# Kernel tuning notes

Hardware: AMD Instinct MI355X
Metric: run time of the kernel (lower is better)

Reference implementation:

```python
import jax, jax.numpy as jnp
import numpy as np

N = 50000          # nodes
E = 800000         # edges (avg degree 16)
IN, H, OUT = 128, 256, 128
K = 100            # low-rank attention rank (hard-coded self.k = 100)
BN_EPS = 1e-5


def _lin(key, din, dout):
    return jax.random.normal(key, (din, dout), jnp.float32) / np.sqrt(din)


def setup_inputs() -> dict:
    key = jax.random.key(0)
    ks = jax.random.split(key, 16)
    inp = {
        "x": jax.random.normal(ks[0], (N, IN), jnp.float32),
        "edge_index": jax.random.randint(ks[1], (2, E), 0, N, jnp.int32),
    }
    dins = [IN, H, H]
    douts = [H, H, OUT]
    j = 2
    for i, (di, do) in enumerate(zip(dins, douts)):
        inp[f"cw{i}"] = _lin(ks[j], di, H); j += 1          # GCNConv weight
        inp[f"cb{i}"] = jnp.zeros((H,), jnp.float32)          # GCNConv bias
        inp[f"aw{i}"] = _lin(ks[j], di, 4 * K); j += 1        # attention U|V|Z|T projection
        inp[f"ab{i}"] = jnp.zeros((4 * K,), jnp.float32)
        inp[f"rw{i}"] = _lin(ks[j], 2 * K + H, do); j += 1    # dimension_reduce linear
        inp[f"rb{i}"] = jnp.zeros((do,), jnp.float32)
    for i in range(2):                                        # BN for first num_layers-1 blocks
        inp[f"g{i}"] = jnp.ones((H,), jnp.float32)
        inp[f"bt{i}"] = jnp.zeros((H,), jnp.float32)
    return inp


def _gcn(x, W, b, src, dst):
    n = x.shape[0]
    loops = jnp.arange(n, dtype=src.dtype)
    s = jnp.concatenate([src, loops])
    d = jnp.concatenate([dst, loops])
    deg = jax.ops.segment_sum(jnp.ones(d.shape, x.dtype), d, num_segments=n)
    dis = jax.lax.rsqrt(jnp.maximum(deg, 1.0))  # deg >= 1 due to self loops
    h = x @ W                                    # [N, H]
    msg = h[s] * (dis[s] * dis[d])[:, None]      # [E+N, H]
    return jax.ops.segment_sum(msg, d, num_segments=n) + b


def _lowrank(x, Aw, Ab):
    # LowRankAttention: tmp = relu(x W); split into U,V,Z,T of width K each.
    t = jax.nn.relu(x @ Aw + Ab)                 # [N, 4K]
    U, V, Z, T = t[:, :K], t[:, K:2 * K], t[:, 2 * K:3 * K], t[:, 3 * K:]
    n = x.shape[0]
    # joint_normalize2: scalar norm factor
    nf = jnp.sum(U @ (V.T @ jnp.ones((n, 1), x.dtype))) / n + 1e-6
    res = U @ (V.T @ Z)                          # low-rank global attention [N, K]
    return jnp.concatenate([res / nf, T], axis=1)  # [N, 2K]


def _bn(x, g, b):
    m = jnp.mean(x, axis=0)
    v = jnp.var(x, axis=0)
    return (x - m) * jax.lax.rsqrt(v + BN_EPS) * g + b


def reference(x, edge_index, cw0, cb0, aw0, ab0, rw0, rb0, g0, bt0,
              cw1, cb1, aw1, ab1, rw1, rb1, g1, bt1,
              cw2, cb2, aw2, ab2, rw2, rb2):
    src, dst = edge_index[0], edge_index[1]
    layers = [(cw0, cb0, aw0, ab0, rw0, rb0, g0, bt0),
              (cw1, cb1, aw1, ab1, rw1, rb1, g1, bt1)]
    for cw, cb, aw, ab, rw, rb, g, bt in layers:
        x_local = jax.nn.relu(_gcn(x, cw, cb, src, dst))  # dropout p=0 (eval)
        x_global = _lowrank(x, aw, ab)
        x = jax.nn.relu(jnp.concatenate([x_global, x_local], axis=1) @ rw + rb)
        x = _bn(x, g, bt)
    x_local = jax.nn.relu(_gcn(x, cw2, cb2, src, dst))
    x_global = _lowrank(x, aw2, ab2)
    return jnp.concatenate([x_global, x_local], axis=1) @ rw2 + rb2
```

## Files before the change

### kernel.cpp

```cpp
#include <hip/hip_runtime.h>

typedef _Float16 f16;
typedef __attribute__((ext_vector_type(8))) _Float16 f16x8;
typedef __attribute__((ext_vector_type(4))) _Float16 f16x4;
typedef __attribute__((ext_vector_type(2))) _Float16 f16x2;
typedef __attribute__((ext_vector_type(4))) float f32x4;

#define LDA2 72

__global__ __launch_bounds__(256, 2) void gemm2(
    const f16* __restrict__ A, int lda,
    const f16* __restrict__ Bt, int Kd,
    const float* __restrict__ bias,
    f16* __restrict__ Cb, float* __restrict__ Cf, int ldc,
    int R, int ncols, int relu,
    float* __restrict__ csbuf,
    float* __restrict__ bnsum_ptr,
    f16* __restrict__ hbD, f16* __restrict__ tbufD, f16* __restrict__ xcatD,
    int mode)
{
    __shared__ f16 As[256 * LDA2];
    __shared__ f16 Bs[128 * LDA2];
    const int tid  = threadIdx.x;
    const int wid  = tid >> 6;
    const int lane = tid & 63;
    const int m    = lane & 15;
    const int quad = lane >> 4;

    const long rowblk = (long)blockIdx.x * 256;
    const long row0   = rowblk + wid * 64;
    const int  colbase = blockIdx.y * 128;

    f32x4 acc[4][8];
#pragma unroll
    for (int rt = 0; rt < 4; ++rt)
#pragma unroll
        for (int ct = 0; ct < 8; ++ct)
            acc[rt][ct] = f32x4{0.f, 0.f, 0.f, 0.f};

    for (int k0 = 0; k0 < Kd; k0 += 64) {
        const int BK = (Kd - k0 >= 64) ? 64 : (Kd - k0);
        const int sb = (BK == 64) ? 3 : 2;
        const int smask = (1 << sb) - 1;
        if (k0) __syncthreads();
        const int itA = BK >> 3;
        for (int i = 0; i < itA; ++i) {
            int u = i * 256 + tid;
            int r = u >> sb, s = u & smask;
            long rr = rowblk + r; if (rr > (long)R - 1) rr = (long)R - 1;
            *(f16x8*)&As[r * LDA2 + s * 8] = *(const f16x8*)(A + rr * (long)lda + k0 + s * 8);
        }
        const int itB = BK >> 4;
        for (int i = 0; i < itB; ++i) {
            int u = i * 256 + tid;
            int c = u >> sb, s = u & smask;
            *(f16x8*)&Bs[c * LDA2 + s * 8] =
                *(const f16x8*)(Bt + (long)(colbase + c) * Kd + k0 + s * 8);
        }
        __syncthreads();
#pragma unroll 2
        for (int kk = 0; kk < BK; kk += 32) {
            f16x8 a[4], b[8];
#pragma unroll
            for (int rt = 0; rt < 4; ++rt)
                a[rt] = *(const f16x8*)&As[(wid * 64 + rt * 16 + m) * LDA2 + kk + quad * 8];
#pragma unroll
            for (int ct = 0; ct < 8; ++ct)
                b[ct] = *(const f16x8*)&Bs[(ct * 16 + m) * LDA2 + kk + quad * 8];
#pragma unroll
            for (int ct = 0; ct < 8; ++ct)
#pragma unroll
                for (int rt = 0; rt < 4; ++rt)
                    acc[rt][ct] = __builtin_amdgcn_mfma_f32_16x16x32_f16(a[rt], b[ct], acc[rt][ct], 0, 0, 0);
        }
    }

    float rsum[8], rsq[8];
#pragma unroll
    for (int ct = 0; ct < 8; ++ct) { rsum[ct] = 0.f; rsq[ct] = 0.f; }

    if (mode == 1) {
#pragma unroll
        for (int ct = 0; ct < 8; ++ct) {
            int col = colbase + ct * 16 + m;
            if (col >= 656) continue;
            float bv = bias[col];
            bool isrelu = col >= 256;
            f16* dst; int ldc2, c2;
            if (col < 256)      { dst = hbD;   ldc2 = 256; c2 = col; }
            else if (col < 556) { dst = tbufD; ldc2 = 300; c2 = col - 256; }
            else                { dst = xcatD; ldc2 = 456; c2 = col - 556; }
#pragma unroll
            for (int rt = 0; rt < 4; ++rt) {
#pragma unroll
                for (int r = 0; r < 4; ++r) {
                    long row = row0 + rt * 16 + quad * 4 + r;
                    if (row < R) {
                        float v = acc[rt][ct][r] + bv;
                        if (isrelu && v < 0.f) v = 0.f;
                        dst[row * (long)ldc2 + c2] = (f16)v;
                        rsum[ct] += v;
                    }
                }
            }
        }
        if (colbase == 256 || colbase == 384) {
            __syncthreads();
            float* scr = (float*)Bs;
#pragma unroll
            for (int ct = 0; ct < 8; ++ct) {
                float s = rsum[ct];
                s += __shfl_xor(s, 16);
                s += __shfl_xor(s, 32);
                if (quad == 0) scr[wid * 128 + ct * 16 + m] = s;
            }
            __syncthreads();
            if (tid < 128) {
                int gcol = colbase + tid;
                if (gcol < 456) {
                    float s = scr[tid] + scr[128 + tid] + scr[256 + tid] + scr[384 + tid];
                    atomicAdd(&csbuf[gcol - 256], s);
                }
            }
        }
    } else {
#pragma unroll
        for (int ct = 0; ct < 8; ++ct) {
            int col = colbase + ct * 16 + m;
            if (col >= ncols) continue;
            float bv = bias ? bias[col] : 0.f;
#pragma unroll
            for (int rt = 0; rt < 4; ++rt) {
#pragma unroll
                for (int r = 0; r < 4; ++r) {
                    long row = row0 + rt * 16 + quad * 4 + r;
                    if (row < R) {
                        float v = acc[rt][ct][r] + bv;
                        if (relu && v < 0.f) v = 0.f;
                        if (Cf) Cf[row * (long)ldc + col] = v;
                        else    Cb[row * (long)ldc + col] = (f16)v;
                        rsum[ct] += v;
                        rsq[ct]  += v * v;
                    }
                }
            }
        }
        if (bnsum_ptr) {
            __syncthreads();
            float* scr = (float*)Bs;
#pragma unroll
            for (int ct = 0; ct < 8; ++ct) {
                float s = rsum[ct];
                s += __shfl_xor(s, 16);
                s += __shfl_xor(s, 32);
                float q = rsq[ct];
                q += __shfl_xor(q, 16);
                q += __shfl_xor(q, 32);
                if (quad == 0) {
                    scr[wid * 128 + ct * 16 + m]       = s;
                    scr[512 + wid * 128 + ct * 16 + m] = q;
                }
            }
            __syncthreads();
            if (tid < 128) {
                int col = colbase + tid;
                if (col < ncols) {
                    float s = scr[tid] + scr[128 + tid] + scr[256 + tid] + scr[384 + tid];
                    float q = scr[512 + tid] + scr[640 + tid] + scr[768 + tid] + scr[896 + tid];
                    atomicAdd(&bnsum_ptr[col], s);
                    atomicAdd(&bnsum_ptr[256 + col], q);
                }
            }
        }
    }
}

struct PrepJobs {
    const float* src[13];
    void*        dst[13];
    int   K[13], ncols[13], Kd[13], type[13];
    long  start[13], elems[13];
    int   njobs;
};

__global__ __launch_bounds__(256) void prep_all(PrepJobs J)
{
    long b = blockIdx.x;
    int j = 0;
    for (int i = 1; i < J.njobs; ++i)
        if (b >= J.start[i]) j = i;
    long idx = (b - J.start[j]) * 256 + threadIdx.x;
    if (idx >= J.elems[j]) return;
    int ty = J.type[j];
    if (ty == 0) {
        int Kd = J.Kd[j];
        int k = (int)(idx % Kd);
        long n = idx / Kd;
        float v = (k < J.K[j] && n < J.ncols[j]) ? J.src[j][(long)k * J.ncols[j] + n] : 0.f;
        ((f16*)J.dst[j])[idx] = (f16)v;
    } else if (ty == 1) {
        ((f16*)J.dst[j])[idx] = (f16)J.src[j][idx];
    } else if (ty == 2) {
        ((float*)J.dst[j])[idx] = 0.f;
    } else {
        float v = (idx >= 256 && idx < 656) ? J.src[j][idx - 256] : 0.f;
        ((float*)J.dst[j])[idx] = v;
    }
}

__global__ void hist_kernel(const int* __restrict__ dst, int E, int* __restrict__ cnt)
{
    int e = blockIdx.x * 256 + threadIdx.x;
    if (e < E) atomicAdd(&cnt[dst[e]], 1);
}

__global__ __launch_bounds__(1024) void scanA_kernel(const int* __restrict__ cnt, int n,
                                                     int* __restrict__ csum)
{
    __shared__ int sdata[1024];
    int t = threadIdx.x;
    int i = blockIdx.x * 1024 + t;
    sdata[t] = (i < n) ? cnt[i] : 0;
    __syncthreads();
    for (int d = 512; d > 0; d >>= 1) {
        if (t < d) sdata[t] += sdata[t + d];
        __syncthreads();
    }
    if (t == 0) csum[blockIdx.x] = sdata[0];
}

__global__ void scanB_kernel(int* __restrict__ csum, int nchunks, int n, int* __restrict__ rowptr)
{
    if (threadIdx.x == 0) {
        int run = 0;
        for (int b = 0; b < nchunks; ++b) {
            int v = csum[b];
            csum[b] = run;
            run += v;
        }
        rowptr[n] = run;
    }
}

__global__ __launch_bounds__(1024) void scanC_kernel(const int* __restrict__ cnt, int n,
                                                     const int* __restrict__ csum,
                                                     int* __restrict__ rowptr,
                                                     int* __restrict__ cursor,
                                                     float* __restrict__ dis)
{
    __shared__ int sdata[1024];
    int t = threadIdx.x;
    int i = blockIdx.x * 1024 + t;
    int v = (i < n) ? cnt[i] : 0;
    sdata[t] = v;
    __syncthreads();
    for (int d = 1; d < 1024; d <<= 1) {
        int x = (t >= d) ? sdata[t - d] : 0;
        __syncthreads();
        sdata[t] += x;
        __syncthreads();
    }
    if (i < n) {
        int excl = csum[blockIdx.x] + sdata[t] - v;
        rowptr[i] = excl;
        cursor[i] = excl;
        dis[i] = rsqrtf((float)(v + 1));
    }
}

__global__ void scatter_kernel(const int* __restrict__ src, const int* __restrict__ dst,
                               int E, int* __restrict__ cursor, int* __restrict__ colidx)
{
    int e = blockIdx.x * 256 + threadIdx.x;
    if (e < E) {
        int d = dst[e];
        int pos = atomicAdd(&cursor[d], 1);
        colidx[pos] = src[e];
    }
}

__global__ __launch_bounds__(256) void agg_kernel(
    const f16* __restrict__ h, const int* __restrict__ rowptr,
    const int* __restrict__ colidx, const float* __restrict__ dis,
    const float* __restrict__ cb, f16* __restrict__ out, int ldc, int R)
{
    int wid = threadIdx.x >> 6, lane = threadIdx.x & 63;
    int i = blockIdx.x * 4 + wid;
    if (i >= R) return;
    float disi = dis[i];
    f16x4 hv = *(const f16x4*)(h + (long)i * 256 + lane * 4);
    float acc[4];
#pragma unroll
    for (int j = 0; j < 4; ++j) acc[j] = (float)hv[j] * disi;
    int e0 = rowptr[i], e1 = rowptr[i + 1];
    int e = e0;
    for (; e + 3 < e1; e += 4) {
        int s0 = colidx[e], s1 = colidx[e + 1], s2 = colidx[e + 2], s3 = colidx[e + 3];
        float w0 = dis[s0], w1 = dis[s1], w2 = dis[s2], w3 = dis[s3];
        f16x4 h0 = *(const f16x4*)(h + (long)s0 * 256 + lane * 4);
        f16x4 h1 = *(const f16x4*)(h + (long)s1 * 256 + lane * 4);
        f16x4 h2 = *(const f16x4*)(h + (long)s2 * 256 + lane * 4);
        f16x4 h3 = *(const f16x4*)(h + (long)s3 * 256 + lane * 4);
#pragma unroll
        for (int j = 0; j < 4; ++j)
            acc[j] += (float)h0[j] * w0 + (float)h1[j] * w1
                    + (float)h2[j] * w2 + (float)h3[j] * w3;
    }
    for (; e < e1; ++e) {
        int s = colidx[e];
        float w = dis[s];
        f16x4 hs = *(const f16x4*)(h + (long)s * 256 + lane * 4);
#pragma unroll
        for (int j = 0; j < 4; ++j) acc[j] += (float)hs[j] * w;
    }
    f16x4 o;
#pragma unroll
    for (int j = 0; j < 4; ++j) {
        float v = acc[j] * disi + cb[lane * 4 + j];
        if (v < 0.f) v = 0.f;
        o[j] = (f16)v;
    }
    *(f16x4*)(out + (long)i * ldc + lane * 4) = o;
}

#define VTZ_BLOCKS 192
__global__ __launch_bounds__(256) void vtz_mfma(const f16* __restrict__ t, int ld, int R,
                                                float* __restrict__ Mpart)
{
    __shared__ f16 Vt[112 * 72];
    __shared__ f16 Zt[112 * 72];
    const int tid  = threadIdx.x;
    const int wid  = tid >> 6;
    const int lane = tid & 63;
    const int m    = lane & 15;
    const int quad = lane >> 4;

    for (int idx = tid; idx < 12 * 64; idx += 256) {
        int c = 100 + (idx >> 6), r = idx & 63;
        Vt[c * 72 + r] = (f16)0.f;
        Zt[c * 72 + r] = (f16)0.f;
    }

    f32x4 acc[2][7];
#pragma unroll
    for (int rt = 0; rt < 2; ++rt)
#pragma unroll
        for (int ct = 0; ct < 7; ++ct)
            acc[rt][ct] = f32x4{0.f, 0.f, 0.f, 0.f};

    for (long base = (long)blockIdx.x * 64; base < R; base += (long)gridDim.x * 64) {
        __syncthreads();
        for (int idx = tid; idx < 50 * 64; idx += 256) {
            int r = idx / 50, c2 = (idx - r * 50) * 2;
            f16x2 v2 = f16x2{(f16)0.f, (f16)0.f};
            f16x2 z2 = f16x2{(f16)0.f, (f16)0.f};
            if (base + r < R) {
                v2 = *(const f16x2*)(t + (base + r) * ld + 100 + c2);
                z2 = *(const f16x2*)(t + (base + r) * ld + 200 + c2);
            }
            Vt[c2 * 72 + r] = v2[0]; Vt[(c2 + 1) * 72 + r] = v2[1];
            Zt[c2 * 72 + r] = z2[0]; Zt[(c2 + 1) * 72 + r] = z2[1];
        }
        __syncthreads();
#pragma unroll
        for (int ks = 0; ks < 2; ++ks) {
            int k0 = ks * 32 + quad * 8;
            f16x8 b[7];
#pragma unroll
            for (int ct = 0; ct < 7; ++ct)
                b[ct] = *(const f16x8*)&Zt[(ct * 16 + m) * 72 + k0];
#pragma unroll
            for (int rt = 0; rt < 2; ++rt) {
                int tr = wid + rt * 4;
                if (tr >= 7) continue;
                f16x8 a = *(const f16x8*)&Vt[(tr * 16 + m) * 72 + k0];
#pragma unroll
                for (int ct = 0; ct < 7; ++ct)
                    acc[rt][ct] = __builtin_amdgcn_mfma_f32_16x16x32_f16(a, b[ct], acc[rt][ct], 0, 0, 0);
            }
        }
    }

    float* out = Mpart + (long)blockIdx.x * 10000;
#pragma unroll
    for (int rt = 0; rt < 2; ++rt) {
        int tr = wid + rt * 4;
        if (tr >= 7) continue;
#pragma unroll
        for (int ct = 0; ct < 7; ++ct) {
            int b = ct * 16 + m;
            if (b >= 100) continue;
#pragma unroll
            for (int r = 0; r < 4; ++r) {
                int a = tr * 16 + quad * 4 + r;
                if (a < 100) out[a * 100 + b] = acc[rt][ct][r];
            }
        }
    }
}

__global__ __launch_bounds__(256) void vtz_reduce2(const float* __restrict__ Mpart,
                                                   f16* __restrict__ MT,
                                                   const float* __restrict__ cs, int R)
{
    __shared__ float s2[256];
    int t = threadIdx.x;
    float v = (t < 100) ? cs[t] * cs[100 + t] : 0.f;
    s2[t] = v;
    __syncthreads();
    for (int d = 128; d > 0; d >>= 1) {
        if (t < d) s2[t] += s2[t + d];
        __syncthreads();
    }
    float scale = 1.0f / (s2[0] / (float)R + 1e-6f);

    int idx = blockIdx.x * 256 + t;
    if (idx >= 10000) return;
    float s = 0.f;
    for (int b = 0; b < VTZ_BLOCKS; ++b) s += Mpart[(long)b * 10000 + idx];
    s *= scale;
    int a = idx / 100, c = idx - a * 100;
    MT[c * 128 + a] = (f16)s;
}

__global__ __launch_bounds__(256) void bn_fold2(
    f16* __restrict__ bigBT,
    const float* __restrict__ cwf, const float* __restrict__ awf,
    const float* __restrict__ bnsum, const float* __restrict__ g,
    const float* __restrict__ bt, int R,
    const float* __restrict__ ab0, float* __restrict__ biascat)
{
    __shared__ float a_s[256], b_s[256];
    const int t = threadIdx.x;
    {
        float s0 = bnsum[t];
        float s1 = bnsum[256 + t];
        float mean = s0 / (float)R;
        float var  = s1 / (float)R - mean * mean;
        if (var < 0.f) var = 0.f;
        float a = g[t] * rsqrtf(var + 1e-5f);
        a_s[t] = a;
        b_s[t] = bt[t] - mean * a;
    }
    __syncthreads();
    const int bid = blockIdx.x;
    if (bid < 768) {
        long idx = (long)bid * 256 + t;
        bigBT[idx] = (f16)((float)bigBT[idx] * a_s[t]);
    } else if (bid == 768) {
        float s = 0.f;
        for (int k = 0; k < 256; ++k) s += b_s[k] * cwf[(long)k * 256 + t];
        biascat[t] = s;
    } else {
        int n = (bid - 769) * 256 + t;
        if (n < 400) {
            float s = ab0[n];
            for (int k = 0; k < 256; ++k) s += b_s[k] * awf[(long)k * 400 + n];
            biascat[256 + n] = s;
        }
    }
}

extern "C" void kernel_launch(void* const* d_in, const int* in_sizes, int n_in,
                              void* d_out, int out_size, void* d_ws, size_t ws_size,
                              hipStream_t stream)
{
    (void)n_in; (void)out_size; (void)ws_size;
    const int N = in_sizes[0] / 128;
    const int E = in_sizes[1] / 2;

    const float* x0 = (const float*)d_in[0];
    const int*  ei   = (const int*)d_in[1];
    const int*  esrc = ei;
    const int*  edst = ei + E;
    const float *cw[3], *cbv[3], *aw[3], *abv[3], *rw[3], *rbv[3];
    for (int l = 0; l < 3; ++l) {
        cw[l]  = (const float*)d_in[2 + 6 * l];
        cbv[l] = (const float*)d_in[3 + 6 * l];
        aw[l]  = (const float*)d_in[4 + 6 * l];
        abv[l] = (const float*)d_in[5 + 6 * l];
        rw[l]  = (const float*)d_in[6 + 6 * l];
        rbv[l] = (const float*)d_in[7 + 6 * l];
    }
    const float* g[2]   = {(const float*)d_in[20], (const float*)d_in[22]};
    const float* btb[2] = {(const float*)d_in[21], (const float*)d_in[23]};

    char* p = (char*)d_ws;
    auto carve = [&](size_t bytes) -> char* {
        char* r = p; p += (bytes + 255) & ~(size_t)255; return r;
    };
    int*   cnt    = (int*)carve((size_t)N * 4);
    int*   rowptr = (int*)carve((size_t)(N + 1) * 4);
    int*   cursor = (int*)carve((size_t)N * 4);
    int*   colidx = (int*)carve((size_t)E * 4);
    float* dis    = (float*)carve((size_t)N * 4);
    int*   csum   = (int*)carve(256 * 4);
    float* Mpart  = (float*)carve((size_t)VTZ_BLOCKS * 10000 * 4);
    float* zr     = (float*)carve(9984 * 4);
    float* csbufL[3] = {zr, zr + 256, zr + 512};
    float* bnsumA = zr + 768;
    float* bnsumB = zr + 1280;
    f16*   MT     = (f16*)(zr + 1792);
    float* biascat = (float*)carve(768 * 4);
    f16*   bigBT[3], *rwT[3];
    int din[3] = {128, 256, 256};
    int dou[3] = {256, 256, 128};
    for (int l = 0; l < 3; ++l) {
        bigBT[l] = (f16*)carve((size_t)768 * din[l] * 2);
        rwT[l]   = (f16*)carve((size_t)dou[l] * 480 * 2);
    }
    f16*   xbf  = (f16*)carve((size_t)N * 256 * 2);
    float* hbuf = (float*)carve((size_t)N * 256 * 4);
    f16*   hb   = (f16*)hbuf;
    f16*   tbuf = (f16*)carve((size_t)N * 300 * 2);
    f16*   xcat = (f16*)carve(((size_t)N * 456 + 32) * 2);

    PrepJobs J{};
    int nj = 0; long blk = 0;
    auto addJob = [&](const float* s, void* d, int K, int nc, int Kd, int ty, long elems) {
        J.src[nj] = s; J.dst[nj] = d; J.K[nj] = K; J.ncols[nj] = nc; J.Kd[nj] = Kd;
        J.type[nj] = ty; J.start[nj] = blk; J.elems[nj] = elems;
        blk += (elems + 255) / 256; ++nj;
    };
    for (int l = 0; l < 3; ++l)
        addJob(cw[l], bigBT[l], din[l], 256, din[l], 0, (long)256 * din[l]);
    for (int l = 0; l < 3; ++l)
        addJob(aw[l], bigBT[l] + (long)256 * din[l], din[l], 400, din[l], 0, (long)512 * din[l]);
    for (int l = 0; l < 3; ++l)
        addJob(rw[l], rwT[l], 456, dou[l], 480, 0, (long)dou[l] * 480);
    addJob(x0, xbf, 0, 0, 0, 1, (long)N * 128);
    addJob(nullptr, zr, 0, 0, 0, 2, 9984);
    addJob(nullptr, cnt, 0, 0, 0, 2, N);
    addJob(abv[0], biascat, 0, 0, 0, 3, 768);
    J.njobs = nj;

    prep_all<<<(unsigned)blk, 256, 0, stream>>>(J);

    const int nchunks = (N + 1023) / 1024;
    hist_kernel<<<(E + 255) / 256, 256, 0, stream>>>(edst, E, cnt);
    scanA_kernel<<<nchunks, 1024, 0, stream>>>(cnt, N, csum);
    scanB_kernel<<<1, 64, 0, stream>>>(csum, nchunks, N, rowptr);
    scanC_kernel<<<nchunks, 1024, 0, stream>>>(cnt, N, csum, rowptr, cursor, dis);
    scatter_kernel<<<(E + 255) / 256, 256, 0, stream>>>(esrc, edst, E, cursor, colidx);

    int lda = 128;
    const unsigned gx2 = (unsigned)((N + 255) / 256);

    for (int l = 0; l < 3; ++l) {
        float* bnsumX = (l == 0) ? bnsumA : bnsumB;

        gemm2<<<dim3(gx2, 6), 256, 0, stream>>>(xbf, lda, bigBT[l], din[l], biascat,
                                                nullptr, nullptr, 0, N, 656, 0,
                                                csbufL[l], nullptr,
                                                hb, tbuf, xcat + 100, 1);
        vtz_mfma<<<VTZ_BLOCKS, 256, 0, stream>>>(tbuf, 300, N, Mpart);
        vtz_reduce2<<<40, 256, 0, stream>>>(Mpart, MT, csbufL[l], N);
        gemm2<<<dim3(gx2, 1), 256, 0, stream>>>(tbuf, 300, MT, 128, nullptr,
                                                xcat, nullptr, 456, N, 100, 0,
                                                nullptr, nullptr,
                                                nullptr, nullptr, nullptr, 0);
        agg_kernel<<<(N + 3) / 4, 256, 0, stream>>>(hb, rowptr, colidx, dis, cbv[l],
                                                    xcat + 200, 456, N);
        if (l < 2) {
            gemm2<<<dim3(gx2, 2), 256, 0, stream>>>(xcat, 456, rwT[l], 480, rbv[l],
                                                    xbf, nullptr, 256, N, 256, 1,
                                                    nullptr, bnsumX,
                                                    nullptr, nullptr, nullptr, 0);
            bn_fold2<<<771, 256, 0, stream>>>(bigBT[l + 1], cw[l + 1], aw[l + 1],
                                              bnsumX, g[l], btb[l], N,
                                              abv[l + 1], biascat);
            lda = 256;
        } else {
            gemm2<<<dim3(gx2, 1), 256, 0, stream>>>(xcat, 456, rwT[l], 480, rbv[l],
                                                    nullptr, (float*)d_out, 128, N, 128, 0,
                                                    nullptr, nullptr,
                                                    nullptr, nullptr, nullptr, 0);
        }
    }
}
```

Before: 980.2 us.

## Register-prefetch GEMM K-tiles and stage epilogue through LDS for vector stores

The GEMM kernel now works on 32-wide K tiles. While the current tile's MFMAs run, the next tile's global loads are already in flight in registers, a register-level software pipeline. The f16 output epilogue first writes results to a per-wave LDS tile, then issues coalesced 4-wide vector stores instead of scattered scalar 2-byte stores. Shared memory is reorganised into one 70KB buffer and the min-blocks launch bound is dropped, which may lower occupancy and add register pressure.

```diff
diff --git a/kernel.cpp b/kernel.cpp
--- a/kernel.cpp
+++ b/kernel.cpp
@@ -6,9 +6,7 @@
 typedef __attribute__((ext_vector_type(2))) _Float16 f16x2;
 typedef __attribute__((ext_vector_type(4))) float f32x4;
 
-#define LDA2 72
-
-__global__ __launch_bounds__(256, 2) void gemm2(
+__global__ __launch_bounds__(256) void gemm3(
     const f16* __restrict__ A, int lda,
     const f16* __restrict__ Bt, int Kd,
     const float* __restrict__ bias,
@@ -19,8 +17,11 @@
     f16* __restrict__ hbD, f16* __restrict__ tbufD, f16* __restrict__ xcatD,
     int mode)
 {
-    __shared__ f16 As[256 * LDA2];
-    __shared__ f16 Bs[128 * LDA2];
+    __shared__ char smem[71680];
+    f16* As = (f16*)smem;
+    f16* Bs = (f16*)(smem + 20480);
+    float* scr = (float*)(smem + 67584);
+
     const int tid  = threadIdx.x;
     const int wid  = tid >> 6;
     const int lane = tid & 63;
@@ -38,58 +39,69 @@
         for (int ct = 0; ct < 8; ++ct)
             acc[rt][ct] = f32x4{0.f, 0.f, 0.f, 0.f};
 
-    for (int k0 = 0; k0 < Kd; k0 += 64) {
-        const int BK = (Kd - k0 >= 64) ? 64 : (Kd - k0);
-        const int sb = (BK == 64) ? 3 : 2;
-        const int smask = (1 << sb) - 1;
+    const f16* pA[4]; f16* wA[4];
+    const f16* pB[2]; f16* wB[2];
+#pragma unroll
+    for (int i = 0; i < 4; ++i) {
+        int u = i * 256 + tid;
+        int r = u >> 2, s = u & 3;
+        long rr = rowblk + r; if (rr > (long)R - 1) rr = (long)R - 1;
+        pA[i] = A + rr * (long)lda + s * 8;
+        wA[i] = &As[r * 40 + s * 8];
+    }
+#pragma unroll
+    for (int i = 0; i < 2; ++i) {
+        int u = i * 256 + tid;
+        int c = u >> 2, s = u & 3;
+        pB[i] = Bt + (long)(colbase + c) * Kd + s * 8;
+        wB[i] = &Bs[c * 40 + s * 8];
+    }
+
+    f16x8 ra[4], rb[2];
+#pragma unroll
+    for (int i = 0; i < 4; ++i) ra[i] = *(const f16x8*)(pA[i]);
+#pragma unroll
+    for (int i = 0; i < 2; ++i) rb[i] = *(const f16x8*)(pB[i]);
+
+    for (int k0 = 0; k0 < Kd; k0 += 32) {
         if (k0) __syncthreads();
-        const int itA = BK >> 3;
-        for (int i = 0; i < itA; ++i) {
-            int u = i * 256 + tid;
-            int r = u >> sb, s = u & smask;
-            long rr = rowblk + r; if (rr > (long)R - 1) rr = (long)R - 1;
-            *(f16x8*)&As[r * LDA2 + s * 8] = *(const f16x8*)(A + rr * (long)lda + k0 + s * 8);
-        }
-        const int itB = BK >> 4;
-        for (int i = 0; i < itB; ++i) {
-            int u = i * 256 + tid;
-            int c = u >> sb, s = u & smask;
-            *(f16x8*)&Bs[c * LDA2 + s * 8] =
-                *(const f16x8*)(Bt + (long)(colbase + c) * Kd + k0 + s * 8);
-        }
+#pragma unroll
+        for (int i = 0; i < 4; ++i) *(f16x8*)wA[i] = ra[i];
+#pragma unroll
+        for (int i = 0; i < 2; ++i) *(f16x8*)wB[i] = rb[i];
         __syncthreads();
-#pragma unroll 2
-        for (int kk = 0; kk < BK; kk += 32) {
-            f16x8 a[4], b[8];
+        if (k0 + 32 < Kd) {
+#pragma unroll
+            for (int i = 0; i < 4; ++i) ra[i] = *(const f16x8*)(pA[i] + k0 + 32);
+#pragma unroll
+            for (int i = 0; i < 2; ++i) rb[i] = *(const f16x8*)(pB[i] + k0 + 32);
+        }
+        f16x8 a[4], b[8];
+#pragma unroll
+        for (int rt = 0; rt < 4; ++rt)
+            a[rt] = *(const f16x8*)&As[(wid * 64 + rt * 16 + m) * 40 + quad * 8];
+#pragma unroll
+        for (int ct = 0; ct < 8; ++ct)
+            b[ct] = *(const f16x8*)&Bs[(ct * 16 + m) * 40 + quad * 8];
+#pragma unroll
+        for (int ct = 0; ct < 8; ++ct)
 #pragma unroll
             for (int rt = 0; rt < 4; ++rt)
-                a[rt] = *(const f16x8*)&As[(wid * 64 + rt * 16 + m) * LDA2 + kk + quad * 8];
-#pragma unroll
-            for (int ct = 0; ct < 8; ++ct)
-                b[ct] = *(const f16x8*)&Bs[(ct * 16 + m) * LDA2 + kk + quad * 8];
-#pragma unroll
-            for (int ct = 0; ct < 8; ++ct)
-#pragma unroll
-                for (int rt = 0; rt < 4; ++rt)
-                    acc[rt][ct] = __builtin_amdgcn_mfma_f32_16x16x32_f16(a[rt], b[ct], acc[rt][ct], 0, 0, 0);
-        }
-    }
+                acc[rt][ct] = __builtin_amdgcn_mfma_f32_16x16x32_f16(a[rt], b[ct], acc[rt][ct], 0, 0, 0);
+    }
+
+    __syncthreads();
 
     float rsum[8], rsq[8];
 #pragma unroll
     for (int ct = 0; ct < 8; ++ct) { rsum[ct] = 0.f; rsq[ct] = 0.f; }
 
-    if (mode == 1) {
+    if (mode == 0 && Cf) {
 #pragma unroll
         for (int ct = 0; ct < 8; ++ct) {
             int col = colbase + ct * 16 + m;
-            if (col >= 656) continue;
-            float bv = bias[col];
-            bool isrelu = col >= 256;
-            f16* dst; int ldc2, c2;
-            if (col < 256)      { dst = hbD;   ldc2 = 256; c2 = col; }
-            else if (col < 556) { dst = tbufD; ldc2 = 300; c2 = col - 256; }
-            else                { dst = xcatD; ldc2 = 456; c2 = col - 556; }
+            if (col >= ncols) continue;
+            float bv = bias ? bias[col] : 0.f;
 #pragma unroll
             for (int rt = 0; rt < 4; ++rt) {
 #pragma unroll
@@ -97,16 +109,58 @@
                     long row = row0 + rt * 16 + quad * 4 + r;
                     if (row < R) {
                         float v = acc[rt][ct][r] + bv;
-                        if (isrelu && v < 0.f) v = 0.f;
-                        dst[row * (long)ldc2 + c2] = (f16)v;
-                        rsum[ct] += v;
+                        if (relu && v < 0.f) v = 0.f;
+                        Cf[row * (long)ldc + col] = v;
                     }
                 }
             }
         }
+        return;
+    }
+
+    f16* epw = (f16*)smem + wid * (64 * 132);
+
+    if (mode == 1) {
+#pragma unroll
+        for (int ct = 0; ct < 8; ++ct) {
+            int col = colbase + ct * 16 + m;
+            float bv = bias[col];
+            bool isrelu = col >= 256;
+#pragma unroll
+            for (int rt = 0; rt < 4; ++rt) {
+#pragma unroll
+                for (int r = 0; r < 4; ++r) {
+                    long row = row0 + rt * 16 + quad * 4 + r;
+                    float v = acc[rt][ct][r] + bv;
+                    if (isrelu && v < 0.f) v = 0.f;
+                    if (row < R) rsum[ct] += v;
+                    epw[(rt * 16 + quad * 4 + r) * 132 + ct * 16 + m] = (f16)v;
+                }
+            }
+        }
+#pragma unroll
+        for (int it = 0; it < 16; ++it) {
+            int rl = it * 4 + (lane >> 4);
+            int ch = lane & 15;
+            long grow = rowblk + wid * 64 + rl;
+            if (grow >= R) continue;
+            f16x4 v0 = *(const f16x4*)&epw[rl * 132 + ch * 8];
+            f16x4 v1 = *(const f16x4*)&epw[rl * 132 + ch * 8 + 4];
+            int cg = colbase + ch * 8;
+#pragma unroll
+            for (int h = 0; h < 2; ++h) {
+                int c4 = cg + h * 4;
+                f16x4 vv = h ? v1 : v0;
+                f16* dst; int ld2, c2;
+                if (c4 < 256)      { dst = hbD;   ld2 = 256; c2 = c4; }
+                else if (c4 < 556) { dst = tbufD; ld2 = 300; c2 = c4 - 256; }
+                else if (c4 < 656) { dst = xcatD; ld2 = 456; c2 = c4 - 556; }
+                else continue;
+                *(f16x4*)&dst[grow * (long)ld2 + c2] = vv;
+            }
+        }
         if (colbase == 256 || colbase == 384) {
             __syncthreads();
-            float* scr = (float*)Bs;
 #pragma unroll
             for (int ct = 0; ct < 8; ++ct) {
                 float s = rsum[ct];
@@ -127,27 +181,40 @@
 #pragma unroll
         for (int ct = 0; ct < 8; ++ct) {
             int col = colbase + ct * 16 + m;
-            if (col >= ncols) continue;
-            float bv = bias ? bias[col] : 0.f;
+            float bv = (bias && col < ncols) ? bias[col] : 0.f;
 #pragma unroll
             for (int rt = 0; rt < 4; ++rt) {
 #pragma unroll
                 for (int r = 0; r < 4; ++r) {
                     long row = row0 + rt * 16 + quad * 4 + r;
-                    if (row < R) {
-                        float v = acc[rt][ct][r] + bv;
-                        if (relu && v < 0.f) v = 0.f;
-                        if (Cf) Cf[row * (long)ldc + col] = v;
-                        else    Cb[row * (long)ldc + col] = (f16)v;
+                    float v = acc[rt][ct][r] + bv;
+                    if (relu && v < 0.f) v = 0.f;
+                    if (col < ncols && row < R) {
                         rsum[ct] += v;
                         rsq[ct]  += v * v;
                     }
+                    epw[(rt * 16 + quad * 4 + r) * 132 + ct * 16 + m] = (f16)v;
                 }
+            }
+        }
+#pragma unroll
+        for (int it = 0; it < 16; ++it) {
+            int rl = it * 4 + (lane >> 4);
+            int ch = lane & 15;
+            long grow = rowblk + wid * 64 + rl;
+            if (grow >= R) continue;
+            f16x4 v0 = *(const f16x4*)&epw[rl * 132 + ch * 8];
+            f16x4 v1 = *(const f16x4*)&epw[rl * 132 + ch * 8 + 4];
+            int cg = colbase + ch * 8;
+#pragma unroll
+            for (int h = 0; h < 2; ++h) {
+                int c4 = cg + h * 4;
+                if (c4 < ncols)
+                    *(f16x4*)&Cb[grow * (long)ldc + c4] = h ? v1 : v0;
             }
         }
         if (bnsum_ptr) {
             __syncthreads();
-            float* scr = (float*)Bs;
 #pragma unroll
             for (int ct = 0; ct < 8; ++ct) {
                 float s = rsum[ct];
@@ -549,20 +616,20 @@
     for (int l = 0; l < 3; ++l) {
         float* bnsumX = (l == 0) ? bnsumA : bnsumB;
 
-        gemm2<<<dim3(gx2, 6), 256, 0, stream>>>(xbf, lda, bigBT[l], din[l], biascat,
+        gemm3<<<dim3(gx2, 6), 256, 0, stream>>>(xbf, lda, bigBT[l], din[l], biascat,
                                                 nullptr, nullptr, 0, N, 656, 0,
                                                 csbufL[l], nullptr,
                                                 hb, tbuf, xcat + 100, 1);
         vtz_mfma<<<VTZ_BLOCKS, 256, 0, stream>>>(tbuf, 300, N, Mpart);
         vtz_reduce2<<<40, 256, 0, stream>>>(Mpart, MT, csbufL[l], N);
-        gemm2<<<dim3(gx2, 1), 256, 0, stream>>>(tbuf, 300, MT, 128, nullptr,
+        gemm3<<<dim3(gx2, 1), 256, 0, stream>>>(tbuf, 300, MT, 128, nullptr,
                                                 xcat, nullptr, 456, N, 100, 0,
                                                 nullptr, nullptr,
                                                 nullptr, nullptr, nullptr, 0);
         agg_kernel<<<(N + 3) / 4, 256, 0, stream>>>(hb, rowptr, colidx, dis, cbv[l],
                                                     xcat + 200, 456, N);
         if (l < 2) {
-            gemm2<<<dim3(gx2, 2), 256, 0, stream>>>(xcat, 456, rwT[l], 480, rbv[l],
+            gemm3<<<dim3(gx2, 2), 256, 0, stream>>>(xcat, 456, rwT[l], 480, rbv[l],
                                                     xbf, nullptr, 256, N, 256, 1,
                                                     nullptr, bnsumX,
                                                     nullptr, nullptr, nullptr, 0);
@@ -571,7 +638,7 @@
                                               abv[l + 1], biascat);
             lda = 256;
         } else {
-            gemm2<<<dim3(gx2, 1), 256, 0, stream>>>(xcat, 456, rwT[l], 480, rbv[l],
+            gemm3<<<dim3(gx2, 1), 256, 0, stream>>>(xcat, 456, rwT[l], 480, rbv[l],
                                                     nullptr, (float*)d_out, 128, N, 128, 0,
                                                     nullptr, nullptr,
                                                     nullptr, nullptr, nullptr, 0);
```

Result: no change. 962.3 us (-1.8%).

## Shrink GEMM tile to 128x128 with 2x2 warp grid and LDS-staged vector stores

Applied to the files above, without the earlier changes.

Replaces the 256x128 GEMM tile with a 128x128 tile split across a 2x2 arrangement of waves, halving accumulator registers and LDS so launch bounds can allow four blocks per CU, with twice as many blocks in the grid. The f16 epilogue now stages results through shared memory and writes 4-wide vector stores instead of scattered scalar stores. The column-sum and BN-statistic reductions are adapted to the new layout. The cost is lower data reuse per block, more redundant B-tile loads, and an extra LDS round trip in the epilogue.

```diff
diff --git a/kernel.cpp b/kernel.cpp
--- a/kernel.cpp
+++ b/kernel.cpp
@@ -6,9 +6,7 @@
 typedef __attribute__((ext_vector_type(2))) _Float16 f16x2;
 typedef __attribute__((ext_vector_type(4))) float f32x4;
 
-#define LDA2 72
-
-__global__ __launch_bounds__(256, 2) void gemm2(
+__global__ __launch_bounds__(256, 4) void gemm4(
     const f16* __restrict__ A, int lda,
     const f16* __restrict__ Bt, int Kd,
     const float* __restrict__ bias,
@@ -19,157 +17,183 @@
     f16* __restrict__ hbD, f16* __restrict__ tbufD, f16* __restrict__ xcatD,
     int mode)
 {
-    __shared__ f16 As[256 * LDA2];
-    __shared__ f16 Bs[128 * LDA2];
+    __shared__ char smem[36864];
+    f16* As = (f16*)smem;
+    f16* Bs = (f16*)(smem + 18432);
+    float* scr = (float*)(smem + 34816);
+
     const int tid  = threadIdx.x;
     const int wid  = tid >> 6;
     const int lane = tid & 63;
     const int m    = lane & 15;
     const int quad = lane >> 4;
-
-    const long rowblk = (long)blockIdx.x * 256;
-    const long row0   = rowblk + wid * 64;
+    const int wr   = wid >> 1;
+    const int wc   = wid & 1;
+
+    const long rowblk  = (long)blockIdx.x * 128;
     const int  colbase = blockIdx.y * 128;
 
-    f32x4 acc[4][8];
+    f32x4 acc[4][4];
 #pragma unroll
     for (int rt = 0; rt < 4; ++rt)
 #pragma unroll
-        for (int ct = 0; ct < 8; ++ct)
+        for (int ct = 0; ct < 4; ++ct)
             acc[rt][ct] = f32x4{0.f, 0.f, 0.f, 0.f};
 
     for (int k0 = 0; k0 < Kd; k0 += 64) {
         const int BK = (Kd - k0 >= 64) ? 64 : (Kd - k0);
-        const int sb = (BK == 64) ? 3 : 2;
-        const int smask = (1 << sb) - 1;
         if (k0) __syncthreads();
-        const int itA = BK >> 3;
-        for (int i = 0; i < itA; ++i) {
-            int u = i * 256 + tid;
-            int r = u >> sb, s = u & smask;
-            long rr = rowblk + r; if (rr > (long)R - 1) rr = (long)R - 1;
-            *(f16x8*)&As[r * LDA2 + s * 8] = *(const f16x8*)(A + rr * (long)lda + k0 + s * 8);
-        }
-        const int itB = BK >> 4;
-        for (int i = 0; i < itB; ++i) {
-            int u = i * 256 + tid;
-            int c = u >> sb, s = u & smask;
-            *(f16x8*)&Bs[c * LDA2 + s * 8] =
-                *(const f16x8*)(Bt + (long)(colbase + c) * Kd + k0 + s * 8);
+        if (BK == 64) {
+#pragma unroll
+            for (int i = 0; i < 4; ++i) {
+                int u = i * 256 + tid;
+                int r = u >> 3, s = u & 7;
+                long rr = rowblk + r; if (rr > (long)R - 1) rr = (long)R - 1;
+                *(f16x8*)&As[r * 72 + s * 8] = *(const f16x8*)(A + rr * (long)lda + k0 + s * 8);
+            }
+#pragma unroll
+            for (int i = 0; i < 4; ++i) {
+                int u = i * 256 + tid;
+                int c = u >> 3, s = u & 7;
+                *(f16x8*)&Bs[c * 72 + s * 8] =
+                    *(const f16x8*)(Bt + (long)(colbase + c) * Kd + k0 + s * 8);
+            }
+        } else {
+#pragma unroll
+            for (int i = 0; i < 2; ++i) {
+                int u = i * 256 + tid;
+                int r = u >> 2, s = u & 3;
+                long rr = rowblk + r; if (rr > (long)R - 1) rr = (long)R - 1;
+                *(f16x8*)&As[r * 72 + s * 8] = *(const f16x8*)(A + rr * (long)lda + k0 + s * 8);
+            }
+#pragma unroll
+            for (int i = 0; i < 2; ++i) {
+                int u = i * 256 + tid;
+                int c = u >> 2, s = u & 3;
+                *(f16x8*)&Bs[c * 72 + s * 8] =
+                    *(const f16x8*)(Bt + (long)(colbase + c) * Kd + k0 + s * 8);
+            }
         }
         __syncthreads();
 #pragma unroll 2
         for (int kk = 0; kk < BK; kk += 32) {
-            f16x8 a[4], b[8];
+            f16x8 a[4], b[4];
 #pragma unroll
             for (int rt = 0; rt < 4; ++rt)
-                a[rt] = *(const f16x8*)&As[(wid * 64 + rt * 16 + m) * LDA2 + kk + quad * 8];
-#pragma unroll
-            for (int ct = 0; ct < 8; ++ct)
-                b[ct] = *(const f16x8*)&Bs[(ct * 16 + m) * LDA2 + kk + quad * 8];
-#pragma unroll
-            for (int ct = 0; ct < 8; ++ct)
+                a[rt] = *(const f16x8*)&As[(wr * 64 + rt * 16 + m) * 72 + kk + quad * 8];
+#pragma unroll
+            for (int ct = 0; ct < 4; ++ct)
+                b[ct] = *(const f16x8*)&Bs[(wc * 64 + ct * 16 + m) * 72 + kk + quad * 8];
+#pragma unroll
+            for (int ct = 0; ct < 4; ++ct)
 #pragma unroll
                 for (int rt = 0; rt < 4; ++rt)
                     acc[rt][ct] = __builtin_amdgcn_mfma_f32_16x16x32_f16(a[rt], b[ct], acc[rt][ct], 0, 0, 0);
         }
     }
 
-    float rsum[8], rsq[8];
-#pragma unroll
-    for (int ct = 0; ct < 8; ++ct) { rsum[ct] = 0.f; rsq[ct] = 0.f; }
-
-    if (mode == 1) {
-#pragma unroll
-        for (int ct = 0; ct < 8; ++ct) {
-            int col = colbase + ct * 16 + m;
-            if (col >= 656) continue;
-            float bv = bias[col];
-            bool isrelu = col >= 256;
-            f16* dst; int ldc2, c2;
-            if (col < 256)      { dst = hbD;   ldc2 = 256; c2 = col; }
-            else if (col < 556) { dst = tbufD; ldc2 = 300; c2 = col - 256; }
-            else                { dst = xcatD; ldc2 = 456; c2 = col - 556; }
-#pragma unroll
-            for (int rt = 0; rt < 4; ++rt) {
-#pragma unroll
-                for (int r = 0; r < 4; ++r) {
-                    long row = row0 + rt * 16 + quad * 4 + r;
-                    if (row < R) {
-                        float v = acc[rt][ct][r] + bv;
-                        if (isrelu && v < 0.f) v = 0.f;
-                        dst[row * (long)ldc2 + c2] = (f16)v;
-                        rsum[ct] += v;
-                    }
-                }
-            }
-        }
-        if (colbase == 256 || colbase == 384) {
-            __syncthreads();
-            float* scr = (float*)Bs;
-#pragma unroll
-            for (int ct = 0; ct < 8; ++ct) {
-                float s = rsum[ct];
-                s += __shfl_xor(s, 16);
-                s += __shfl_xor(s, 32);
-                if (quad == 0) scr[wid * 128 + ct * 16 + m] = s;
-            }
-            __syncthreads();
-            if (tid < 128) {
-                int gcol = colbase + tid;
-                if (gcol < 456) {
-                    float s = scr[tid] + scr[128 + tid] + scr[256 + tid] + scr[384 + tid];
-                    atomicAdd(&csbuf[gcol - 256], s);
-                }
-            }
-        }
-    } else {
-#pragma unroll
-        for (int ct = 0; ct < 8; ++ct) {
-            int col = colbase + ct * 16 + m;
+    __syncthreads();
+
+    if (mode == 0 && Cf) {
+#pragma unroll
+        for (int ct = 0; ct < 4; ++ct) {
+            int col = colbase + wc * 64 + ct * 16 + m;
             if (col >= ncols) continue;
             float bv = bias ? bias[col] : 0.f;
 #pragma unroll
             for (int rt = 0; rt < 4; ++rt) {
 #pragma unroll
                 for (int r = 0; r < 4; ++r) {
-                    long row = row0 + rt * 16 + quad * 4 + r;
+                    long row = rowblk + wr * 64 + rt * 16 + quad * 4 + r;
                     if (row < R) {
                         float v = acc[rt][ct][r] + bv;
                         if (relu && v < 0.f) v = 0.f;
-                        if (Cf) Cf[row * (long)ldc + col] = v;
-                        else    Cb[row * (long)ldc + col] = (f16)v;
-                        rsum[ct] += v;
-                        rsq[ct]  += v * v;
+                        Cf[row * (long)ldc + col] = v;
                     }
                 }
             }
         }
-        if (bnsum_ptr) {
-            __syncthreads();
-            float* scr = (float*)Bs;
-#pragma unroll
-            for (int ct = 0; ct < 8; ++ct) {
-                float s = rsum[ct];
-                s += __shfl_xor(s, 16);
-                s += __shfl_xor(s, 32);
-                float q = rsq[ct];
-                q += __shfl_xor(q, 16);
-                q += __shfl_xor(q, 32);
-                if (quad == 0) {
-                    scr[wid * 128 + ct * 16 + m]       = s;
-                    scr[512 + wid * 128 + ct * 16 + m] = q;
+        return;
+    }
+
+    float rsum[4], rsq[4];
+#pragma unroll
+    for (int ct = 0; ct < 4; ++ct) { rsum[ct] = 0.f; rsq[ct] = 0.f; }
+
+    f16* epw = (f16*)smem + wid * (64 * 68);
+
+    const bool needsum = (mode == 1) ? (colbase == 256 || colbase == 384)
+                                     : (bnsum_ptr != nullptr);
+
+#pragma unroll
+    for (int ct = 0; ct < 4; ++ct) {
+        int col = colbase + wc * 64 + ct * 16 + m;
+        float bv;
+        if (mode == 1) bv = bias[col];
+        else           bv = (bias && col < ncols) ? bias[col] : 0.f;
+        bool isrelu = (mode == 1) ? (col >= 256) : (relu != 0);
+#pragma unroll
+        for (int rt = 0; rt < 4; ++rt) {
+#pragma unroll
+            for (int r = 0; r < 4; ++r) {
+                long row = rowblk + wr * 64 + rt * 16 + quad * 4 + r;
+                float v = acc[rt][ct][r] + bv;
+                if (isrelu && v < 0.f) v = 0.f;
+                if (needsum && row < R && col < ((mode == 1) ? 656 : ncols)) {
+                    rsum[ct] += v;
+                    rsq[ct]  += v * v;
                 }
-            }
-            __syncthreads();
-            if (tid < 128) {
-                int col = colbase + tid;
-                if (col < ncols) {
-                    float s = scr[tid] + scr[128 + tid] + scr[256 + tid] + scr[384 + tid];
-                    float q = scr[512 + tid] + scr[640 + tid] + scr[768 + tid] + scr[896 + tid];
-                    atomicAdd(&bnsum_ptr[col], s);
-                    atomicAdd(&bnsum_ptr[256 + col], q);
-                }
+                epw[(rt * 16 + quad * 4 + r) * 68 + ct * 16 + m] = (f16)v;
+            }
+        }
+    }
+
+#pragma unroll
+    for (int it = 0; it < 16; ++it) {
+        int rl = it * 4 + (lane >> 4);
+        int ch = lane & 15;
+        long grow = rowblk + wr * 64 + rl;
+        if (grow >= R) continue;
+        f16x4 vv = *(const f16x4*)&epw[rl * 68 + ch * 4];
+        int c4 = colbase + wc * 64 + ch * 4;
+        if (mode == 1) {
+            f16* dst; int ld2, c2;
+            if (c4 < 256)      { dst = hbD;   ld2 = 256; c2 = c4; }
+            else if (c4 < 556) { dst = tbufD; ld2 = 300; c2 = c4 - 256; }
+            else if (c4 < 656) { dst = xcatD; ld2 = 456; c2 = c4 - 556; }
+            else continue;
+            *(f16x4*)&dst[grow * (long)ld2 + c2] = vv;
+        } else {
+            if (c4 < ncols)
+                *(f16x4*)&Cb[grow * (long)ldc + c4] = vv;
+        }
+    }
+
+    if (needsum) {
+        __syncthreads();
+#pragma unroll
+        for (int ct = 0; ct < 4; ++ct) {
+            float s = rsum[ct];
+            s += __shfl_xor(s, 16);
+            s += __shfl_xor(s, 32);
+            float q = rsq[ct];
+            q += __shfl_xor(q, 16);
+            q += __shfl_xor(q, 32);
+            if (quad == 0) {
+                scr[wr * 128 + wc * 64 + ct * 16 + m]       = s;
+                scr[256 + wr * 128 + wc * 64 + ct * 16 + m] = q;
+            }
+        }
+        __syncthreads();
+        if (tid < 128) {
+            int gcol = colbase + tid;
+            float s = scr[tid] + scr[128 + tid];
+            if (mode == 1) {
+                if (gcol >= 256 && gcol < 456) atomicAdd(&csbuf[gcol - 256], s);
+            } else if (gcol < ncols) {
+                float q = scr[256 + tid] + scr[384 + tid];
+                atomicAdd(&bnsum_ptr[gcol], s);
+                atomicAdd(&bnsum_ptr[256 + gcol], q);
             }
         }
     }
@@ -544,37 +568,37 @@
     scatter_kernel<<<(E + 255) / 256, 256, 0, stream>>>(esrc, edst, E, cursor, colidx);
 
     int lda = 128;
-    const unsigned gx2 = (unsigned)((N + 255) / 256);
+    const unsigned gx = (unsigned)((N + 127) / 128);
 
     for (int l = 0; l < 3; ++l) {
         float* bnsumX = (l == 0) ? bnsumA : bnsumB;
 
-        gemm2<<<dim3(gx2, 6), 256, 0, stream>>>(xbf, lda, bigBT[l], din[l], biascat,
-                                                nullptr, nullptr, 0, N, 656, 0,
-                                                csbufL[l], nullptr,
-                                                hb, tbuf, xcat + 100, 1);
+        gemm4<<<dim3(gx, 6), 256, 0, stream>>>(xbf, lda, bigBT[l], din[l], biascat,
+                                               nullptr, nullptr, 0, N, 656, 0,
+                                               csbufL[l], nullptr,
+                                               hb, tbuf, xcat + 100, 1);
         vtz_mfma<<<VTZ_BLOCKS, 256, 0, stream>>>(tbuf, 300, N, Mpart);
         vtz_reduce2<<<40, 256, 0, stream>>>(Mpart, MT, csbufL[l], N);
-        gemm2<<<dim3(gx2, 1), 256, 0, stream>>>(tbuf, 300, MT, 128, nullptr,
-                                                xcat, nullptr, 456, N, 100, 0,
-                                                nullptr, nullptr,
-                                                nullptr, nullptr, nullptr, 0);
+        gemm4<<<dim3(gx, 1), 256, 0, stream>>>(tbuf, 300, MT, 128, nullptr,
+                                               xcat, nullptr, 456, N, 100, 0,
+                                               nullptr, nullptr,
+                                               nullptr, nullptr, nullptr, 0);
         agg_kernel<<<(N + 3) / 4, 256, 0, stream>>>(hb, rowptr, colidx, dis, cbv[l],
                                                     xcat + 200, 456, N);
         if (l < 2) {
-            gemm2<<<dim3(gx2, 2), 256, 0, stream>>>(xcat, 456, rwT[l], 480, rbv[l],
-                                                    xbf, nullptr, 256, N, 256, 1,
-                                                    nullptr, bnsumX,
-                                                    nullptr, nullptr, nullptr, 0);
+            gemm4<<<dim3(gx, 2), 256, 0, stream>>>(xcat, 456, rwT[l], 480, rbv[l],
+                                                   xbf, nullptr, 256, N, 256, 1,
+                                                   nullptr, bnsumX,
+                                                   nullptr, nullptr, nullptr, 0);
             bn_fold2<<<771, 256, 0, stream>>>(bigBT[l + 1], cw[l + 1], aw[l + 1],
                                               bnsumX, g[l], btb[l], N,
                                               abv[l + 1], biascat);
             lda = 256;
         } else {
-            gemm2<<<dim3(gx2, 1), 256, 0, stream>>>(xcat, 456, rwT[l], 480, rbv[l],
-                                                    nullptr, (float*)d_out, 128, N, 128, 0,
-                                                    nullptr, nullptr,
-                                                    nullptr, nullptr, nullptr, 0);
-        }
-    }
-}
+            gemm4<<<dim3(gx, 1), 256, 0, stream>>>(xcat, 456, rwT[l], 480, rbv[l],
+                                                   nullptr, (float*)d_out, 128, N, 128, 0,
+                                                   nullptr, nullptr,
+                                                   nullptr, nullptr, nullptr, 0);
+        }
+    }
+}
```

Measured after the change: 947.8 us. 1.03x faster.
